# Optimization experiments

Measured on AMD Instinct MI355X. Metric: run time of the kernel, lower is better.

Reference implementation:

```python
import jax, jax.numpy as jnp
import numpy as np
from jax import lax

N_NODES = 8192
N_FEAT = 256
N_EDGES = 131072


def _cc_labels(src, dst, n):
    """Weakly-connected-component labels via min-label propagation + pointer jumping.
    Converged label[i] == min node index in i's component (matches scipy's
    first-occurrence labeling order after compaction)."""
    def cond(state):
        return state[1]

    def body(state):
        label, _ = state
        m = jnp.minimum(label[src], label[dst])
        new = label.at[src].min(m).at[dst].min(m)
        new = new[new]  # pointer jump
        return new, jnp.any(new != label)

    label, _ = lax.while_loop(cond, body, (jnp.arange(n, dtype=jnp.int32), jnp.array(True)))
    return label


def setup_inputs() -> dict:
    key = jax.random.key(0)
    k1, k2, k3 = jax.random.split(key, 3)
    x = jax.random.normal(k1, (N_NODES, N_FEAT), dtype=jnp.float32)
    edge_index = jax.random.randint(k2, (2, N_EDGES), 0, N_NODES, dtype=jnp.int32)
    batch = jnp.zeros((N_NODES,), dtype=jnp.int32)
    lin_w = jax.random.normal(k3, (1, 2 * N_FEAT), dtype=jnp.float32) * 0.05
    lin_b = jnp.zeros((1,), dtype=jnp.float32)
    return {"x": x, "edge_index": edge_index, "batch": batch, "lin_w": lin_w, "lin_b": lin_b}


def reference(x, edge_index, batch, lin_w, lin_b):
    n, f = x.shape
    src, dst = edge_index[0], edge_index[1]
    msk = src != dst  # drop self loops (kept in buffer, zeroed via mask for static shapes)
    # undirected: add flipped edges -> 2E directed edges
    src2 = jnp.concatenate([src, dst])
    dst2 = jnp.concatenate([dst, src])
    m2 = jnp.concatenate([msk, msk])
    mf = m2.astype(x.dtype)

    # edge score: Linear(2F,1) on [x[src] || x[dst]] == x@w1 gathered + x@w2 gathered
    w1, w2 = lin_w[0, :f], lin_w[0, f:]
    p1 = x @ w1  # [N]
    p2 = x @ w2  # [N]
    e = jnp.tanh(p1[src2] + p2[dst2] + lin_b[0])  # [2E]

    # contracted edges: score > threshold (0.0); masked edges excluded
    contract = m2 & (e > 0.0)
    srcc = jnp.where(contract, src2, 0)
    dstc = jnp.where(contract, dst2, 0)
    label = _cc_labels(srcc, dstc, n)
    # compact labels in order of smallest node index per component (== scipy ordering)
    is_root = (label == jnp.arange(n, dtype=label.dtype))
    cluster = (jnp.cumsum(is_root.astype(jnp.int32)) - 1)[label]  # [N], values in [0, K)

    # dense adjacency A and score adjacency S (scatter-add, like to_dense_adj)
    A = jnp.zeros((n, n), x.dtype).at[src2, dst2].add(mf)
    S = jnp.zeros((n, n), x.dtype).at[src2, dst2].add(e * mf)

    # isolated nodes w.r.t. contracted adjacency -> S[i,i] = 1
    cint = contract.astype(jnp.int32)
    deg = jnp.zeros(n, jnp.int32).at[src2].add(cint) + jnp.zeros(n, jnp.int32).at[dst2].add(cint)
    isolated = deg == 0
    idx = jnp.arange(n)
    S = S.at[idx, idx].set(jnp.where(isolated, jnp.ones((), x.dtype), S[idx, idx]))

    # X_new = (S @ C).T @ X = C.T @ (S.T @ X)  -- C.T@ is a segment-sum over clusters
    # (padded to N rows; rows >= num_clusters are zero)
    X_new = jax.ops.segment_sum(S.T @ x, cluster, num_segments=n)

    # coarsened adjacency C.T @ A @ C with zero diagonal (dense, padded to NxN)
    M1 = jax.ops.segment_sum(A, cluster, num_segments=n)        # pool rows
    A_c = jax.ops.segment_sum(M1.T, cluster, num_segments=n).T  # pool cols
    A_c = A_c.at[idx, idx].set(0.0)

    new_batch = jnp.zeros(n, batch.dtype).at[cluster].set(batch)
    return X_new, A_c, new_batch, cluster
```

## Files before the change

### kernel.cpp

```cpp
#include <hip/hip_runtime.h>
#include <math.h>

#define N_NODES 8192
#define N_FEAT  256
#define N_EDGES 131072
#define N_DIR   (2*N_EDGES)
#define MAXDEG  128
#define ACT_CAP 24576

typedef unsigned int u32x4 __attribute__((ext_vector_type(4)));


__device__ __forceinline__ void edge_sd(const int* __restrict__ ei, int k, int& s, int& d){
  s = ei[k];
  d = (k < N_EDGES) ? ei[k + N_EDGES] : ei[k - N_EDGES];
}


__global__ void k_start(int* __restrict__ meta, int nmeta, int* __restrict__ Lg){
  int i = blockIdx.x * blockDim.x + threadIdx.x;
  if (i < nmeta) meta[i] = 0;
  if (i < N_NODES) Lg[i] = i;
}

__global__ void k_proj(const float* __restrict__ x, const float* __restrict__ w,
                       float* __restrict__ p1, float* __restrict__ p2){
  int i = blockIdx.x;
  int t = threadIdx.x;
  float v = x[(size_t)i * N_FEAT + t];
  double a = (double)v * (double)w[t];
  double b = (double)v * (double)w[N_FEAT + t];
  for (int off = 32; off; off >>= 1){
    a += __shfl_down(a, off);
    b += __shfl_down(b, off);
  }
  __shared__ double sa[4], sb[4];
  int wid = t >> 6, lane = t & 63;
  if (lane == 0){ sa[wid] = a; sb[wid] = b; }
  __syncthreads();
  if (t == 0){
    p1[i] = (float)(sa[0] + sa[1] + sa[2] + sa[3]);
    p2[i] = (float)(sb[0] + sb[1] + sb[2] + sb[3]);
  }
}

__global__ void k_edges(const int* __restrict__ ei, const float* __restrict__ p1,
                        const float* __restrict__ p2, const float* __restrict__ lb,
                        int* __restrict__ cnt, int* __restrict__ deg,
                        int* __restrict__ Lg, uint2* __restrict__ edata,
                        unsigned int* __restrict__ pairs, int* __restrict__ np){
  int k = blockIdx.x * blockDim.x + threadIdx.x;
  int s, d; edge_sd(ei, k, s, d);
  bool selfe = (s == d);
  float e = 0.0f;
  if (!selfe){
    float z = p1[s] + p2[d] + lb[0];
    e = tanhf(z);
    int slot = atomicAdd(&cnt[d], 1);
    uint2 v; v.x = (unsigned int)s; v.y = __float_as_uint(e);
    edata[(size_t)d * MAXDEG + slot] = v;
    if (e > 0.0f){
      atomicAdd(&deg[s], 1);
      atomicAdd(&deg[d], 1);
      int hi = s > d ? s : d;
      int lo = s > d ? d : s;
      atomicMin(&Lg[hi], lo);
    }
  }
  bool c = (!selfe) && (e > 0.0f);
  unsigned long long m = __ballot(c);
  if (m){
    int lane = threadIdx.x & 63;
    int leader = __ffsll((unsigned long long)m) - 1;
    int base = 0;
    if (lane == leader) base = atomicAdd(np, __popcll(m));
    base = __shfl(base, leader);
    if (c){
      int prefix = __popcll(m & ((1ull << lane) - 1ull));
      pairs[base + prefix] = ((unsigned int)s << 13) | (unsigned int)d;
    }
  }
}

__global__ void k_flat(int* __restrict__ Lg){
  int i = blockIdx.x * blockDim.x + threadIdx.x;
  if (i >= N_NODES) return;
  int l = Lg[i];
  while (true){ int q = Lg[l]; if (q == l) break; l = q; }
  Lg[i] = l;
}

__global__ void k_relax(const unsigned int* __restrict__ pairs,
                        const int* __restrict__ np, int* __restrict__ Lg){
  int n = *np;
  int k = blockIdx.x * blockDim.x + threadIdx.x;
  int stride = gridDim.x * blockDim.x;
  for (; k < n; k += stride){
    unsigned int p = pairs[k];
    int s = (int)(p >> 13), d = (int)(p & 8191u);
    int a = Lg[s], b = Lg[d];
    if (a < b)      atomicMin(&Lg[d], a);
    else if (b < a) atomicMin(&Lg[s], b);
  }
}

__global__ void k_collect(const unsigned int* __restrict__ pairs,
                          const int* __restrict__ np, const int* __restrict__ Lg,
                          unsigned int* __restrict__ gact, int* __restrict__ ngact){
  int n = *np;
  int k = blockIdx.x * blockDim.x + threadIdx.x;
  int stride = gridDim.x * blockDim.x;
  for (; k < n; k += stride){
    unsigned int p = pairs[k];
    int s = (int)(p >> 13), d = (int)(p & 8191u);
    bool act = (Lg[s] != Lg[d]);
    unsigned long long m = __ballot(act);
    if (m){
      int lane = threadIdx.x & 63;
      int leader = __ffsll((unsigned long long)m) - 1;
      int base = 0;
      if (lane == leader) base = atomicAdd(ngact, __popcll(m));
      base = __shfl(base, leader);
      if (act){
        int prefix = __popcll(m & ((1ull << lane) - 1ull));
        gact[base + prefix] = p;
      }
    }
  }
}

__global__ void __launch_bounds__(1024) k_fused(
    const unsigned int* __restrict__ gact, const int* __restrict__ ngact,
    const int* __restrict__ Lg, const int* __restrict__ batch,
    int* __restrict__ cluster_i, float* __restrict__ out_cluster,
    float* __restrict__ out_batch,
    u32x4* __restrict__ zbase, long long n4){
  int t = threadIdx.x;

  if (blockIdx.x != 0){
    long long i = (long long)(blockIdx.x - 1) * blockDim.x + t;
    long long stride = (long long)(gridDim.x - 1) * blockDim.x;
    u32x4 z = (u32x4)(0u);
    for (; i < n4; i += stride) __builtin_nontemporal_store(z, &zbase[i]);
    return;
  }

  __shared__ int L[N_NODES];
  __shared__ int wsum[1024];
  __shared__ unsigned int act[ACT_CAP];
  __shared__ int flag;

  for (int i = t; i < N_NODES; i += 1024) L[i] = Lg[i];
  for (int i = t; i < N_NODES; i += 1024) out_batch[i] = 0.0f;
  __syncthreads();

  int na = *ngact;
  if (na > 0){
    bool inlds = (na <= ACT_CAP);
    if (inlds){
      for (int k = t; k < na; k += 1024) act[k] = gact[k];
    }
    __syncthreads();
    while (true){
      if (t == 0) flag = 0;
      __syncthreads();
      for (int k = t; k < na; k += 1024){
        unsigned int p = inlds ? act[k] : gact[k];
        int s = (int)(p >> 13), d = (int)(p & 8191u);
        int a = L[s], b = L[d];
        if (a == b) continue;
        int m = a < b ? a : b;
        atomicMin(&L[s], m);
        atomicMin(&L[d], m);
        if (a > m) atomicMin(&L[a], m);
        else       atomicMin(&L[b], m);
        flag = 1;
      }
      __syncthreads();
      if (!flag) break;
      for (int i = t; i < N_NODES; i += 1024){
        int l = L[i];
        while (true){ int q = L[l]; if (q == l) break; l = q; }
        L[i] = l;
      }
      __syncthreads();
    }
  }

  int base = t * 8;
  int l_reg[8];
  #pragma unroll
  for (int j = 0; j < 8; ++j) l_reg[j] = L[base + j];
  __syncthreads();

  int f[8]; int s = 0;
  #pragma unroll
  for (int j = 0; j < 8; ++j){ f[j] = (l_reg[j] == base + j) ? 1 : 0; s += f[j]; }
  wsum[t] = s;
  __syncthreads();
  for (int off = 1; off < 1024; off <<= 1){
    int v = (t >= off) ? wsum[t - off] : 0;
    __syncthreads();
    wsum[t] += v;
    __syncthreads();
  }
  int run = wsum[t] - s;
  #pragma unroll
  for (int j = 0; j < 8; ++j){
    run += f[j];
    if (f[j]) L[base + j] = run - 1;
  }
  __syncthreads();

  #pragma unroll
  for (int j = 0; j < 8; ++j){
    int i = base + j;
    int c = L[l_reg[j]];
    cluster_i[i] = c;
    out_cluster[i] = (float)c;
    out_batch[c] = (float)batch[i];
  }
}

__global__ void k_y(const float* __restrict__ x, const uint2* __restrict__ edata,
                    const int* __restrict__ cnt, const int* __restrict__ deg,
                    float* __restrict__ y){
  int i = blockIdx.x;
  int t = threadIdx.x;
  int m = cnt[i];
  float acc = (deg[i] == 0) ? x[(size_t)i * N_FEAT + t] : 0.0f;
  const uint2* row = edata + (size_t)i * MAXDEG;
  for (int j = 0; j < m; ++j){
    uint2 v = row[j];
    acc += __uint_as_float(v.y) * x[(size_t)v.x * N_FEAT + t];
  }
  y[(size_t)i * N_FEAT + t] = acc;
}

__global__ void k_xnew(const float* __restrict__ y, const int* __restrict__ cluster_i,
                       float* __restrict__ Xn){
  int t = threadIdx.x;
  int node0 = blockIdx.x * 32;
  float acc = 0.0f;
  int cur = cluster_i[node0];
  for (int j = 0; j < 32; ++j){
    int node = node0 + j;
    int c = cluster_i[node];
    if (c != cur){
      atomicAdd(&Xn[(size_t)cur * N_FEAT + t], acc);
      acc = 0.0f; cur = c;
    }
    acc += y[(size_t)node * N_FEAT + t];
  }
  atomicAdd(&Xn[(size_t)cur * N_FEAT + t], acc);
}

__global__ void k_ac(const int* __restrict__ ei, const int* __restrict__ cluster_i,
                     float* __restrict__ Ac){
  int k = blockIdx.x * blockDim.x + threadIdx.x;
  if (k >= N_DIR) return;
  int s, d; edge_sd(ei, k, s, d);
  if (s == d) return;
  int cs = cluster_i[s], cd = cluster_i[d];
  if (cs != cd) atomicAdd(&Ac[(size_t)cs * N_NODES + cd], 1.0f);
}


extern "C" void kernel_launch(void* const* d_in, const int* in_sizes, int n_in,
                              void* d_out, int out_size, void* d_ws, size_t ws_size,
                              hipStream_t stream){
  const float* x     = (const float*)d_in[0];
  const int*   ei    = (const int*)  d_in[1];
  const int*   batch = (const int*)  d_in[2];
  const float* lw    = (const float*)d_in[3];
  const float* lb    = (const float*)d_in[4];

  float* out = (float*)d_out;
  float* Xn  = out;
  float* Ac  = Xn + (size_t)N_NODES * N_FEAT;
  float* ob  = Ac + (size_t)N_NODES * N_NODES;
  float* oc  = ob + N_NODES;

  char* w = (char*)d_ws;
  float* p1        = (float*)w; w += (size_t)N_NODES * 4;
  float* p2        = (float*)w; w += (size_t)N_NODES * 4;
  int*   cluster_i = (int*)  w; w += (size_t)N_NODES * 4;
  int*   Lg        = (int*)  w; w += (size_t)N_NODES * 4;
  int*   meta      = (int*)  w;
  int*   cnt       = meta;
  int*   deg       = meta + N_NODES;
  int*   np        = meta + 2 * N_NODES;
  int*   ngact     = meta + 2 * N_NODES + 1;
  int    nmeta     = 2 * N_NODES + 16;
  w += (size_t)nmeta * 4;
  unsigned int* pairs = (unsigned int*)w; w += (size_t)N_DIR * 4;
  unsigned int* gact  = (unsigned int*)w; w += (size_t)N_DIR * 4;
  uint2* edata     = (uint2*)w; w += (size_t)N_NODES * MAXDEG * 8;
  float* y         = (float*)w; w += (size_t)N_NODES * N_FEAT * 4;

  long long n4 = ((long long)N_NODES * N_FEAT + (long long)N_NODES * N_NODES) / 4;

  k_start  <<<(nmeta + 255) / 256, 256, 0, stream>>>(meta, nmeta, Lg);
  k_proj   <<<N_NODES, 256, 0, stream>>>(x, lw, p1, p2);
  k_edges  <<<N_DIR / 256, 256, 0, stream>>>(ei, p1, p2, lb, cnt, deg, Lg,
                                             edata, pairs, np);
  k_flat   <<<N_NODES / 256, 256, 0, stream>>>(Lg);
  k_relax  <<<512, 256, 0, stream>>>(pairs, np, Lg);
  k_flat   <<<N_NODES / 256, 256, 0, stream>>>(Lg);
  k_collect<<<512, 256, 0, stream>>>(pairs, np, Lg, gact, ngact);
  k_fused  <<<256, 1024, 0, stream>>>(gact, ngact, Lg, batch, cluster_i, oc, ob,
                                      (u32x4*)out, n4);
  k_y      <<<N_NODES, 256, 0, stream>>>(x, edata, cnt, deg, y);
  k_xnew   <<<N_NODES / 32, 256, 0, stream>>>(y, cluster_i, Xn);
  k_ac     <<<N_DIR / 256, 256, 0, stream>>>(ei, cluster_i, Ac);
}
```

Baseline: 279.0 us.

## Fuse active-edge collection into rank kernel and fuse y computation into X_new pooling

The separate collect kernel is removed. Its active-edge filtering now runs inside the single-block rank kernel, which compacts edges into LDS with a shared atomic counter. The y intermediate buffer is eliminated: k_y and k_xnew merge so each block computes the per-node S^T x rows and pools them by cluster directly. Zeroing is redistributed so that Xn is cleared in k_start and Ac is cleared by extra blocks of the fused y/X_new kernel. The costs are that the single-block kernel now scans all pairs serially on one CU, and X_new is computed by only 256 blocks of 32 nodes, which lowers parallelism for the gather work.

```diff
diff --git a/kernel.cpp b/kernel.cpp
--- a/kernel.cpp
+++ b/kernel.cpp
@@ -17,10 +17,14 @@
 }
 
 
-__global__ void k_start(int* __restrict__ meta, int nmeta, int* __restrict__ Lg){
+__global__ void k_start(int* __restrict__ meta, int nmeta, int* __restrict__ Lg,
+                        u32x4* __restrict__ xn4, int nx4){
   int i = blockIdx.x * blockDim.x + threadIdx.x;
   if (i < nmeta) meta[i] = 0;
   if (i < N_NODES) Lg[i] = i;
+  u32x4 z = (u32x4)(0u);
+  int stride = gridDim.x * blockDim.x;
+  for (int k = i; k < nx4; k += stride) __builtin_nontemporal_store(z, &xn4[k]);
 }
 
 __global__ void k_proj(const float* __restrict__ x, const float* __restrict__ w,
@@ -104,68 +108,41 @@
   }
 }
 
-__global__ void k_collect(const unsigned int* __restrict__ pairs,
-                          const int* __restrict__ np, const int* __restrict__ Lg,
-                          unsigned int* __restrict__ gact, int* __restrict__ ngact){
-  int n = *np;
-  int k = blockIdx.x * blockDim.x + threadIdx.x;
-  int stride = gridDim.x * blockDim.x;
-  for (; k < n; k += stride){
-    unsigned int p = pairs[k];
-    int s = (int)(p >> 13), d = (int)(p & 8191u);
-    bool act = (Lg[s] != Lg[d]);
-    unsigned long long m = __ballot(act);
-    if (m){
-      int lane = threadIdx.x & 63;
-      int leader = __ffsll((unsigned long long)m) - 1;
-      int base = 0;
-      if (lane == leader) base = atomicAdd(ngact, __popcll(m));
-      base = __shfl(base, leader);
-      if (act){
-        int prefix = __popcll(m & ((1ull << lane) - 1ull));
-        gact[base + prefix] = p;
-      }
-    }
-  }
-}
-
-__global__ void __launch_bounds__(1024) k_fused(
-    const unsigned int* __restrict__ gact, const int* __restrict__ ngact,
+__global__ void __launch_bounds__(1024) k_rank1(
+    const unsigned int* __restrict__ pairs, const int* __restrict__ np,
     const int* __restrict__ Lg, const int* __restrict__ batch,
     int* __restrict__ cluster_i, float* __restrict__ out_cluster,
-    float* __restrict__ out_batch,
-    u32x4* __restrict__ zbase, long long n4){
-  int t = threadIdx.x;
-
-  if (blockIdx.x != 0){
-    long long i = (long long)(blockIdx.x - 1) * blockDim.x + t;
-    long long stride = (long long)(gridDim.x - 1) * blockDim.x;
-    u32x4 z = (u32x4)(0u);
-    for (; i < n4; i += stride) __builtin_nontemporal_store(z, &zbase[i]);
-    return;
-  }
-
+    float* __restrict__ out_batch){
   __shared__ int L[N_NODES];
   __shared__ int wsum[1024];
   __shared__ unsigned int act[ACT_CAP];
-  __shared__ int flag;
+  __shared__ int nact, flag;
+  int t = threadIdx.x;
 
   for (int i = t; i < N_NODES; i += 1024) L[i] = Lg[i];
   for (int i = t; i < N_NODES; i += 1024) out_batch[i] = 0.0f;
-  __syncthreads();
-
-  int na = *ngact;
+  if (t == 0){ nact = 0; flag = 0; }
+  __syncthreads();
+
+  int n = *np;
+  for (int k = t; k < n; k += 1024){
+    unsigned int p = pairs[k];
+    int s = (int)(p >> 13), d = (int)(p & 8191u);
+    if (L[s] != L[d]){
+      int a = atomicAdd(&nact, 1);
+      if (a < ACT_CAP) act[a] = p;
+    }
+  }
+  __syncthreads();
+  int na = nact;
   if (na > 0){
     bool inlds = (na <= ACT_CAP);
-    if (inlds){
-      for (int k = t; k < na; k += 1024) act[k] = gact[k];
-    }
-    __syncthreads();
+    int mend = inlds ? na : n;
     while (true){
       if (t == 0) flag = 0;
       __syncthreads();
-      for (int k = t; k < na; k += 1024){
-        unsigned int p = inlds ? act[k] : gact[k];
+      for (int k = t; k < mend; k += 1024){
+        unsigned int p = inlds ? act[k] : pairs[k];
         int s = (int)(p >> 13), d = (int)(p & 8191u);
         int a = L[s], b = L[d];
         if (a == b) continue;
@@ -222,35 +199,36 @@
   }
 }
 
-__global__ void k_y(const float* __restrict__ x, const uint2* __restrict__ edata,
-                    const int* __restrict__ cnt, const int* __restrict__ deg,
-                    float* __restrict__ y){
-  int i = blockIdx.x;
+__global__ void k_yx(const float* __restrict__ x, const uint2* __restrict__ edata,
+                     const int* __restrict__ cnt, const int* __restrict__ deg,
+                     const int* __restrict__ cluster_i, float* __restrict__ Xn,
+                     u32x4* __restrict__ ac4, long long na4){
   int t = threadIdx.x;
-  int m = cnt[i];
-  float acc = (deg[i] == 0) ? x[(size_t)i * N_FEAT + t] : 0.0f;
-  const uint2* row = edata + (size_t)i * MAXDEG;
-  for (int j = 0; j < m; ++j){
-    uint2 v = row[j];
-    acc += __uint_as_float(v.y) * x[(size_t)v.x * N_FEAT + t];
-  }
-  y[(size_t)i * N_FEAT + t] = acc;
-}
-
-__global__ void k_xnew(const float* __restrict__ y, const int* __restrict__ cluster_i,
-                       float* __restrict__ Xn){
-  int t = threadIdx.x;
+  if (blockIdx.x >= 256){
+    long long i = (long long)(blockIdx.x - 256) * blockDim.x + t;
+    long long stride = (long long)(gridDim.x - 256) * blockDim.x;
+    u32x4 z = (u32x4)(0u);
+    for (; i < na4; i += stride) __builtin_nontemporal_store(z, &ac4[i]);
+    return;
+  }
   int node0 = blockIdx.x * 32;
   float acc = 0.0f;
   int cur = cluster_i[node0];
   for (int j = 0; j < 32; ++j){
-    int node = node0 + j;
-    int c = cluster_i[node];
+    int i = node0 + j;
+    int c = cluster_i[i];
     if (c != cur){
       atomicAdd(&Xn[(size_t)cur * N_FEAT + t], acc);
       acc = 0.0f; cur = c;
     }
-    acc += y[(size_t)node * N_FEAT + t];
+    float yv = (deg[i] == 0) ? x[(size_t)i * N_FEAT + t] : 0.0f;
+    int m = cnt[i];
+    const uint2* row = edata + (size_t)i * MAXDEG;
+    for (int j2 = 0; j2 < m; ++j2){
+      uint2 v = row[j2];
+      yv += __uint_as_float(v.y) * x[(size_t)v.x * N_FEAT + t];
+    }
+    acc += yv;
   }
   atomicAdd(&Xn[(size_t)cur * N_FEAT + t], acc);
 }
@@ -290,27 +268,23 @@
   int*   cnt       = meta;
   int*   deg       = meta + N_NODES;
   int*   np        = meta + 2 * N_NODES;
-  int*   ngact     = meta + 2 * N_NODES + 1;
   int    nmeta     = 2 * N_NODES + 16;
   w += (size_t)nmeta * 4;
   unsigned int* pairs = (unsigned int*)w; w += (size_t)N_DIR * 4;
-  unsigned int* gact  = (unsigned int*)w; w += (size_t)N_DIR * 4;
   uint2* edata     = (uint2*)w; w += (size_t)N_NODES * MAXDEG * 8;
-  float* y         = (float*)w; w += (size_t)N_NODES * N_FEAT * 4;
-
-  long long n4 = ((long long)N_NODES * N_FEAT + (long long)N_NODES * N_NODES) / 4;
-
-  k_start  <<<(nmeta + 255) / 256, 256, 0, stream>>>(meta, nmeta, Lg);
-  k_proj   <<<N_NODES, 256, 0, stream>>>(x, lw, p1, p2);
-  k_edges  <<<N_DIR / 256, 256, 0, stream>>>(ei, p1, p2, lb, cnt, deg, Lg,
-                                             edata, pairs, np);
-  k_flat   <<<N_NODES / 256, 256, 0, stream>>>(Lg);
-  k_relax  <<<512, 256, 0, stream>>>(pairs, np, Lg);
-  k_flat   <<<N_NODES / 256, 256, 0, stream>>>(Lg);
-  k_collect<<<512, 256, 0, stream>>>(pairs, np, Lg, gact, ngact);
-  k_fused  <<<256, 1024, 0, stream>>>(gact, ngact, Lg, batch, cluster_i, oc, ob,
-                                      (u32x4*)out, n4);
-  k_y      <<<N_NODES, 256, 0, stream>>>(x, edata, cnt, deg, y);
-  k_xnew   <<<N_NODES / 32, 256, 0, stream>>>(y, cluster_i, Xn);
-  k_ac     <<<N_DIR / 256, 256, 0, stream>>>(ei, cluster_i, Ac);
-}
+
+  int nx4 = (N_NODES * N_FEAT) / 4;
+  long long na4 = ((long long)N_NODES * N_NODES) / 4;
+
+  k_start <<<2048, 256, 0, stream>>>(meta, nmeta, Lg, (u32x4*)Xn, nx4);
+  k_proj  <<<N_NODES, 256, 0, stream>>>(x, lw, p1, p2);
+  k_edges <<<N_DIR / 256, 256, 0, stream>>>(ei, p1, p2, lb, cnt, deg, Lg,
+                                            edata, pairs, np);
+  k_flat  <<<N_NODES / 256, 256, 0, stream>>>(Lg);
+  k_relax <<<512, 256, 0, stream>>>(pairs, np, Lg);
+  k_flat  <<<N_NODES / 256, 256, 0, stream>>>(Lg);
+  k_rank1 <<<1, 1024, 0, stream>>>(pairs, np, Lg, batch, cluster_i, oc, ob);
+  k_yx    <<<256 + 1024, 256, 0, stream>>>(x, edata, cnt, deg, cluster_i, Xn,
+                                           (u32x4*)Ac, na4);
+  k_ac    <<<N_DIR / 256, 256, 0, stream>>>(ei, cluster_i, Ac);
+}
```

Measured after the change: 504.1 us. 1.81x slower.
